# Performance work log

Measured on AMD Instinct MI355X. Metric: run time of the kernel, lower is better.

The kernel has to match this reference:

```python
import jax, jax.numpy as jnp
import numpy as np

EMBED_DIM = 1280
NUM_HEADS = 32
HEAD_DIM = EMBED_DIM // NUM_HEADS  # 40
SCALING = HEAD_DIM ** -0.5
BSZ, TGT_LEN, PAST_LEN = 2, 1024, 1024


def setup_inputs() -> dict:
    key = jax.random.key(0)
    ks = jax.random.split(key, 8)
    w_scale = 1.0 / np.sqrt(EMBED_DIM)
    return {
        "inputs": jax.random.normal(ks[0], (BSZ, TGT_LEN, EMBED_DIM), jnp.float32),
        "past_key": jax.random.normal(ks[1], (BSZ, NUM_HEADS, PAST_LEN, HEAD_DIM), jnp.float32),
        "past_value": jax.random.normal(ks[2], (BSZ, NUM_HEADS, PAST_LEN, HEAD_DIM), jnp.float32),
        "Wq": jax.random.normal(ks[3], (EMBED_DIM, EMBED_DIM), jnp.float32) * w_scale,
        "bq": jnp.zeros((EMBED_DIM,), jnp.float32),
        "Wk": jax.random.normal(ks[4], (EMBED_DIM, EMBED_DIM), jnp.float32) * w_scale,
        "bk": jnp.zeros((EMBED_DIM,), jnp.float32),
        "Wv": jax.random.normal(ks[5], (EMBED_DIM, EMBED_DIM), jnp.float32) * w_scale,
        "bv": jnp.zeros((EMBED_DIM,), jnp.float32),
        "Wo": jax.random.normal(ks[6], (EMBED_DIM, EMBED_DIM), jnp.float32) * w_scale,
        "bo": jnp.zeros((EMBED_DIM,), jnp.float32),
    }


def _shape(x, bsz):
    # [b, s, e] -> [b, h, s, d]
    return x.reshape(bsz, -1, NUM_HEADS, HEAD_DIM).transpose(0, 2, 1, 3)


def reference(inputs, past_key, past_value, Wq, bq, Wk, bk, Wv, bv, Wo, bo):
    bsz, tgt_len, _ = inputs.shape
    # projections (dropout rate is 0 -> identity)
    q = _shape((inputs @ Wq + bq) * SCALING, bsz)        # [b,h,t,d]
    k_new = _shape(inputs @ Wk + bk, bsz)                # [b,h,t,d]
    v_new = _shape(inputs @ Wv + bv, bsz)
    # KV-cache concat along seq axis
    key_states = jnp.concatenate([past_key, k_new], axis=2)    # [b,h,s,d]
    value_states = jnp.concatenate([past_value, v_new], axis=2)
    # attention: QK^T -> softmax -> AV (full score matrix, as original)
    attn_weights = jnp.einsum('bhid,bhjd->bhij', q, key_states)  # [b,h,t,s]
    attn_probs = jax.nn.softmax(attn_weights, axis=-1)
    attn_output = jnp.einsum('bhij,bhjd->bhid', attn_probs, value_states)  # [b,h,t,d]
    attn_output = attn_output.transpose(0, 2, 1, 3).reshape(bsz, tgt_len, EMBED_DIM)
    attn_output = attn_output @ Wo + bo
    return attn_output, key_states, value_states
```

## Files before the change

### kernel.cpp

```cpp
#include <hip/hip_runtime.h>
#include <hip/hip_bf16.h>

#define ED 1280
#define NH 32
#define HD 40
#define BSZ 2
#define TL 1024
#define SEQ 2048
#define SCALING 0.15811388300841897f

typedef __bf16 bf16x8 __attribute__((ext_vector_type(8)));
typedef float floatx4 __attribute__((ext_vector_type(4)));
typedef unsigned short ushort;
typedef ushort ushortx8 __attribute__((ext_vector_type(8)));

__device__ __forceinline__ ushort f2bf(float f) {
    __hip_bfloat16 h = __float2bfloat16(f);
    return *(ushort*)&h;
}
__device__ __forceinline__ unsigned pk2(float a, float b) {
    return (unsigned)f2bf(a) | ((unsigned)f2bf(b) << 16);
}

#define ASYNC16(g, l)                                                                 \
    __builtin_amdgcn_global_load_lds((const __attribute__((address_space(1))) void*)(g), \
                                     (__attribute__((address_space(3))) void*)(l), 16, 0, 0)

__global__ void convert_x_zero(const float* X, ushort* Xb, ushort* Qb) {
    int bid = blockIdx.x;
    if (bid < 2560) {
        int i = (bid * 256 + threadIdx.x) * 4;
        float4 v = *(const float4*)&X[i];
        ushort4 o;
        o.x = f2bf(v.x); o.y = f2bf(v.y); o.z = f2bf(v.z); o.w = f2bf(v.w);
        *(ushort4*)&Xb[i] = o;
    } else {
        int i = ((bid - 2560) * 256 + threadIdx.x) * 8;
        uint4 z = {0, 0, 0, 0};
        *(uint4*)&Qb[i] = z;
    }
}

__global__ void transpose_w(const float* w0, const float* w1,
                            const float* w2, const float* w3, ushort* wt) {
    __shared__ float tile[32][33];
    int z = blockIdx.z;
    const float* w = (z == 0) ? w0 : (z == 1) ? w1 : (z == 2) ? w2 : w3;
    ushort* o = wt + (size_t)z * ED * ED;
    int n0 = blockIdx.x * 32, k0 = blockIdx.y * 32;
    int tx = threadIdx.x, ty = threadIdx.y;
#pragma unroll
    for (int i = ty; i < 32; i += 8) tile[i][tx] = w[(k0 + i) * ED + n0 + tx];
    __syncthreads();
#pragma unroll
    for (int i = ty; i < 32; i += 8) o[(n0 + i) * ED + k0 + tx] = f2bf(tile[tx][i]);
}

__global__ void copy_past(const float* PK, const float* PV, float* keyOut, float* valOut) {
    int idx = blockIdx.x * 256 + threadIdx.x;
    int which = idx >= 655360;
    int f4 = which ? idx - 655360 : idx;
    const float4* src = (const float4*)(which ? PV : PK);
    float4* dst = (float4*)(which ? valOut : keyOut);
    int bhj = f4 / 10, c4 = f4 - bhj * 10;
    int bh = bhj >> 10, j = bhj & 1023;
    dst[(bh * SEQ + j) * 10 + c4] = src[f4];
}

__global__ void prep_k(const float* keyOut, ushort* Kb16) {
    int idx = blockIdx.x * 256 + threadIdx.x;
    int row = idx / 6, j = idx - row * 6;
    uint4 o = {0, 0, 0, 0};
    if (j < 5) {
        const float* s = &keyOut[(size_t)row * 40 + j * 8];
        float4 a = *(const float4*)s;
        float4 b = *(const float4*)(s + 4);
        o.x = pk2(a.x, a.y); o.y = pk2(a.z, a.w);
        o.z = pk2(b.x, b.y); o.w = pk2(b.z, b.w);
    }
    *(uint4*)&Kb16[(size_t)row * 48 + j * 8] = o;
}

__global__ void prep_v(const float* valOut, ushort* Vt16) {
    __shared__ ushort T[48 * 72];
    int bh = blockIdx.x, st = blockIdx.y;
    int tid = threadIdx.x;
    for (int i = tid; i < 8 * 72; i += 256) {
        int dr = i / 72, k = i - dr * 72;
        T[(40 + dr) * 72 + k] = (dr == 0) ? 0x3F80 : 0;
    }
    const float* src = valOut + ((size_t)bh * SEQ + st * 64) * 40;
    for (int i = tid; i < 640; i += 256) {
        int key = i / 10, c = i - key * 10;
        float4 v = *(const float4*)&src[key * 40 + c * 4];
        T[(c * 4 + 0) * 72 + key] = f2bf(v.x);
        T[(c * 4 + 1) * 72 + key] = f2bf(v.y);
        T[(c * 4 + 2) * 72 + key] = f2bf(v.z);
        T[(c * 4 + 3) * 72 + key] = f2bf(v.w);
    }
    __syncthreads();
    ushort* dst = Vt16 + (size_t)bh * 48 * 2048 + st * 64;
    for (int i = tid; i < 384; i += 256) {
        int d = i >> 3, c = i & 7;
        *(uint4*)&dst[(size_t)d * 2048 + c * 8] = *(const uint4*)&T[d * 72 + c * 8];
    }
}

__device__ __forceinline__ void gemm_core_db(const ushort* A, const ushort* Bt,
                                             ushort* As, ushort* Bs,
                                             int m0, int n0, floatx4 acc[4][2]) {
    int tidx = threadIdx.x;
    int wave = tidx >> 6, lane = tidx & 63;
    int wm = (wave >> 1) * 64, wn = (wave & 1) * 32;
    int fr = lane & 15, kq = lane >> 4;
    int fa = tidx * 8, ra = fa >> 5, ca = fa & 31;
    const ushort* a0 = &A[(m0 + ra) * ED + ca];
    const ushort* a1 = &A[(m0 + 64 + ra) * ED + ca];
    const ushort* bsrc = &Bt[(n0 + ra) * ED + ca];
    ASYNC16(a0, &As[fa]);
    ASYNC16(a1, &As[2048 + fa]);
    ASYNC16(bsrc, &Bs[fa]);
    __syncthreads();
    for (int k0 = 0; k0 < ED; k0 += 32) {
        int cur = (k0 >> 5) & 1;
        if (k0 + 32 < ED) {
            int nxt = cur ^ 1;
            ASYNC16(a0 + k0 + 32, &As[nxt * 4096 + fa]);
            ASYNC16(a1 + k0 + 32, &As[nxt * 4096 + 2048 + fa]);
            ASYNC16(bsrc + k0 + 32, &Bs[nxt * 2048 + fa]);
        }
        bf16x8 a[4], b[2];
#pragma unroll
        for (int mi = 0; mi < 4; ++mi)
            a[mi] = *(const bf16x8*)&As[cur * 4096 + (wm + mi * 16 + fr) * 32 + kq * 8];
#pragma unroll
        for (int ni = 0; ni < 2; ++ni)
            b[ni] = *(const bf16x8*)&Bs[cur * 2048 + (wn + ni * 16 + fr) * 32 + kq * 8];
#pragma unroll
        for (int mi = 0; mi < 4; ++mi)
#pragma unroll
            for (int ni = 0; ni < 2; ++ni)
                acc[mi][ni] = __builtin_amdgcn_mfma_f32_16x16x32_bf16(a[mi], b[ni], acc[mi][ni], 0, 0, 0);
        __syncthreads();
    }
}

__global__ __launch_bounds__(256) void gemm_qkv(const ushort* Xb, const ushort* Wt,
                                                const float* bq, const float* bk,
                                                const float* bv, ushort* Qb,
                                                float* keyOut, float* valOut) {
    __shared__ ushort As[2 * 128 * 32], Bs[2 * 64 * 32];
    int z = blockIdx.z;
    const ushort* Bt = Wt + (size_t)z * ED * ED;
    const float* bias = (z == 0) ? bq : (z == 1) ? bk : bv;
    int m0 = blockIdx.y * 128, n0 = blockIdx.x * 64;
    floatx4 acc[4][2] = {};
    gemm_core_db(Xb, Bt, As, Bs, m0, n0, acc);
    int lane = threadIdx.x & 63, wave = threadIdx.x >> 6;
    int wm = (wave >> 1) * 64, wn = (wave & 1) * 32;
    int cq = lane >> 4, cc = lane & 15;
#pragma unroll
    for (int mi = 0; mi < 4; ++mi)
#pragma unroll
        for (int ni = 0; ni < 2; ++ni) {
            int col = n0 + wn + ni * 16 + cc;
            float bvf = bias[col];
            int h = col / HD, dh = col - h * HD;
#pragma unroll
            for (int r = 0; r < 4; ++r) {
                int row = m0 + wm + mi * 16 + cq * 4 + r;
                int b = row >> 10, t = row & 1023;
                float v = acc[mi][ni][r] + bvf;
                if (z == 0) {
                    Qb[(((b * NH + h) * TL) + t) * 64 + dh] = f2bf(v * SCALING);
                } else {
                    int idx = ((b * NH + h) * SEQ + TL + t) * HD + dh;
                    (z == 1 ? keyOut : valOut)[idx] = v;
                }
            }
        }
}

__global__ __launch_bounds__(256) void gemm_out(const ushort* A, const ushort* Bt,
                                                const float* bias, float* out) {
    __shared__ ushort As[2 * 128 * 32], Bs[2 * 64 * 32];
    int m0 = blockIdx.y * 128, n0 = blockIdx.x * 64;
    floatx4 acc[4][2] = {};
    gemm_core_db(A, Bt, As, Bs, m0, n0, acc);
    int lane = threadIdx.x & 63, wave = threadIdx.x >> 6;
    int wm = (wave >> 1) * 64, wn = (wave & 1) * 32;
    int cq = lane >> 4, cc = lane & 15;
#pragma unroll
    for (int mi = 0; mi < 4; ++mi)
#pragma unroll
        for (int ni = 0; ni < 2; ++ni) {
            int col = n0 + wn + ni * 16 + cc;
            float bvf = bias[col];
#pragma unroll
            for (int r = 0; r < 4; ++r) {
                int row = m0 + wm + mi * 16 + cq * 4 + r;
                out[row * ED + col] = acc[mi][ni][r] + bvf;
            }
        }
}

__global__ __launch_bounds__(256) void attn_mfma(const ushort* Qb, const ushort* Kb16,
                                                 const ushort* Vt16, ushort* O) {
    __shared__ ushort Ks[2 * 64 * 64];
    __shared__ ushort Vs[2 * 48 * 64];

    int bh = blockIdx.x, b = bh >> 5, h = bh & 31;
    int tid = threadIdx.x, wave = tid >> 6, lane = tid & 63;
    int col = lane & 15, quad = lane >> 4;
    int qbase = blockIdx.y * 64 + wave * 16;

    bf16x8 qa[2];
#pragma unroll
    for (int ks = 0; ks < 2; ++ks)
        qa[ks] = *(const bf16x8*)(Qb + ((size_t)bh * TL + qbase + col) * 64 + ks * 32 + quad * 8);

    const ushort* ksrc[2];
    int kinc[2];
#pragma unroll
    for (int u = 0; u < 2; ++u) {
        int j = u * 256 + tid;
        int srow = j >> 3, ci = j & 7;
        int dch = ci ^ (srow & 7);
        int key = 32 * (srow >> 5) + 8 * ((srow >> 2) & 3) + 4 * ((srow >> 4) & 1) + (srow & 3);
        bool data = dch < 6;
        ksrc[u] = data ? Kb16 + ((size_t)bh * SEQ + key) * 48 + dch * 8 : Qb + 48;
        kinc[u] = data ? 64 * 48 : 0;
    }
    const ushort* vsrc[2];
#pragma unroll
    for (int u = 0; u < 2; ++u) {
        int j = u * 256 + tid;
        int row = j >> 3, ci = j & 7;
        int dch = ci ^ (row & 7);
        vsrc[u] = Vt16 + (size_t)bh * 48 * SEQ + (size_t)(row < 48 ? row : 0) * SEQ + dch * 8;
    }

    floatx4 Oacc[3] = {};
    int kxor = (col & 7) << 3;

#pragma unroll
    for (int u = 0; u < 2; ++u) {
        ASYNC16(ksrc[u], &Ks[(u * 256 + tid) * 8]);
        ksrc[u] += kinc[u];
    }
    ASYNC16(vsrc[0], &Vs[tid * 8]);
    vsrc[0] += 64;
    if (tid < 128) {
        ASYNC16(vsrc[1], &Vs[(256 + tid) * 8]);
        vsrc[1] += 64;
    }
    __syncthreads();

#pragma unroll 1
    for (int t = 0; t < SEQ / 64; ++t) {
        ushort* KsC = Ks + (t & 1) * (64 * 64);
        ushort* VsC = Vs + (t & 1) * (48 * 64);
        if (t + 1 < SEQ / 64) {
            ushort* KsN = Ks + ((t + 1) & 1) * (64 * 64);
            ushort* VsN = Vs + ((t + 1) & 1) * (48 * 64);
#pragma unroll
            for (int u = 0; u < 2; ++u) {
                ASYNC16(ksrc[u], &KsN[(u * 256 + tid) * 8]);
                ksrc[u] += kinc[u];
            }
            ASYNC16(vsrc[0], &VsN[tid * 8]);
            vsrc[0] += 64;
            if (tid < 128) {
                ASYNC16(vsrc[1], &VsN[(256 + tid) * 8]);
                vsrc[1] += 64;
            }
        }

        __builtin_amdgcn_s_setprio(1);
        floatx4 S[4] = {};
#pragma unroll
        for (int ks = 0; ks < 2; ++ks)
#pragma unroll
            for (int n = 0; n < 4; ++n) {
                int row = n * 16 + col;
                bf16x8 kb = *(const bf16x8*)&KsC[row * 64 + (((ks * 4 + quad) << 3) ^ kxor)];
                S[n] = __builtin_amdgcn_mfma_f32_16x16x32_bf16(kb, qa[ks], S[n], 0, 0, 0);
            }

#pragma unroll
        for (int ks = 0; ks < 2; ++ks) {
            unsigned w[4];
#pragma unroll
            for (int pi = 0; pi < 4; ++pi) {
                int i0 = pi * 2, i1 = i0 + 1;
                float s0 = S[2 * ks + (i0 >> 2)][i0 & 3];
                float s1 = S[2 * ks + (i1 >> 2)][i1 & 3];
                unsigned b0 = (unsigned)(int)fmaf(s0, 184.6649652f, 14035.0f);
                unsigned b1 = (unsigned)(int)fmaf(s1, 184.6649652f, 14035.0f);
                w[pi] = b0 | (b1 << 16);
            }
            uint4 pw;
            pw.x = w[0]; pw.y = w[1]; pw.z = w[2]; pw.w = w[3];
            bf16x8 pa = __builtin_bit_cast(bf16x8, pw);
            int c = ks * 4 + quad;
            int cpos = (c << 3) ^ kxor;
#pragma unroll
            for (int no = 0; no < 3; ++no) {
                int row = no * 16 + col;
                bf16x8 vb = *(const bf16x8*)&VsC[row * 64 + cpos];
                Oacc[no] = __builtin_amdgcn_mfma_f32_16x16x32_bf16(pa, vb, Oacc[no], 0, 0, 0);
            }
        }
        __builtin_amdgcn_s_setprio(0);

        __syncthreads();
    }

    float linv[4];
#pragma unroll
    for (int r = 0; r < 4; ++r)
        linv[r] = 1.f / __shfl(Oacc[2][r], (lane & 48) + 8, 64);
#pragma unroll
    for (int n = 0; n < 3; ++n) {
        int d = n * 16 + col;
        if (d < HD) {
#pragma unroll
            for (int r = 0; r < 4; ++r) {
                int q = qbase + quad * 4 + r;
                O[(size_t)(b * TL + q) * ED + h * HD + d] = f2bf(Oacc[n][r] * linv[r]);
            }
        }
    }
}

extern "C" void kernel_launch(void* const* d_in, const int* in_sizes, int n_in,
                              void* d_out, int out_size, void* d_ws, size_t ws_size,
                              hipStream_t stream) {
    const float* X  = (const float*)d_in[0];
    const float* PK = (const float*)d_in[1];
    const float* PV = (const float*)d_in[2];
    const float* Wq = (const float*)d_in[3];
    const float* bq = (const float*)d_in[4];
    const float* Wk = (const float*)d_in[5];
    const float* bk = (const float*)d_in[6];
    const float* Wv = (const float*)d_in[7];
    const float* bv = (const float*)d_in[8];
    const float* Wo = (const float*)d_in[9];
    const float* bo = (const float*)d_in[10];

    float* out = (float*)d_out;
    float* keyOut = out + 2621440;
    float* valOut = keyOut + 5242880;

    ushort* ws   = (ushort*)d_ws;
    ushort* Wt   = ws;
    ushort* Qb   = Wt + 4 * (ED * ED);
    ushort* Kb16 = Qb + (size_t)65536 * 64;
    ushort* Vt16 = Kb16 + (size_t)131072 * 48;
    ushort* Xb   = Vt16 + (size_t)64 * 48 * 2048;
    ushort* Aws  = Xb;

    convert_x_zero<<<dim3(4608), dim3(256), 0, stream>>>(X, Xb, Qb);
    transpose_w<<<dim3(40, 40, 4), dim3(32, 8), 0, stream>>>(Wq, Wk, Wv, Wo, Wt);
    copy_past<<<dim3(5120), dim3(256), 0, stream>>>(PK, PV, keyOut, valOut);
    gemm_qkv<<<dim3(20, 16, 3), dim3(256), 0, stream>>>(Xb, Wt, bq, bk, bv, Qb, keyOut, valOut);
    prep_k<<<dim3(3072), dim3(256), 0, stream>>>(keyOut, Kb16);
    prep_v<<<dim3(64, 32), dim3(256), 0, stream>>>(valOut, Vt16);
    attn_mfma<<<dim3(64, 16), dim3(256), 0, stream>>>(Qb, Kb16, Vt16, Aws);
    gemm_out<<<dim3(20, 16), dim3(256), 0, stream>>>(Aws, Wt + 3 * (ED * ED), bo, out);
}
```

Baseline: 240.1 us.

## Fuse past KV copy with bf16 K/V packing and emit new K/V from QKV GEMM

Replaces the separate copy_past, prep_k and prep_v kernels with one prep_past kernel. It copies the past key/value into the output cache and writes the bf16 padded K and transposed V buffers in the same pass. The QKV GEMM epilogue now also writes the new-token K rows and transposed V columns in bf16 directly. This removes two kernel launches and a re-read of the fp32 key/value caches, at the cost of extra scattered 2-byte stores in the GEMM epilogue.

```diff
diff --git a/kernel.cpp b/kernel.cpp
--- a/kernel.cpp
+++ b/kernel.cpp
@@ -17,9 +17,6 @@
 __device__ __forceinline__ ushort f2bf(float f) {
     __hip_bfloat16 h = __float2bfloat16(f);
     return *(ushort*)&h;
-}
-__device__ __forceinline__ unsigned pk2(float a, float b) {
-    return (unsigned)f2bf(a) | ((unsigned)f2bf(b) << 16);
 }
 
 #define ASYNC16(g, l)                                                                 \
@@ -56,53 +53,57 @@
     for (int i = ty; i < 32; i += 8) o[(n0 + i) * ED + k0 + tx] = f2bf(tile[tx][i]);
 }
 
-__global__ void copy_past(const float* PK, const float* PV, float* keyOut, float* valOut) {
-    int idx = blockIdx.x * 256 + threadIdx.x;
-    int which = idx >= 655360;
-    int f4 = which ? idx - 655360 : idx;
-    const float4* src = (const float4*)(which ? PV : PK);
-    float4* dst = (float4*)(which ? valOut : keyOut);
-    int bhj = f4 / 10, c4 = f4 - bhj * 10;
-    int bh = bhj >> 10, j = bhj & 1023;
-    dst[(bh * SEQ + j) * 10 + c4] = src[f4];
-}
-
-__global__ void prep_k(const float* keyOut, ushort* Kb16) {
-    int idx = blockIdx.x * 256 + threadIdx.x;
-    int row = idx / 6, j = idx - row * 6;
-    uint4 o = {0, 0, 0, 0};
-    if (j < 5) {
-        const float* s = &keyOut[(size_t)row * 40 + j * 8];
-        float4 a = *(const float4*)s;
-        float4 b = *(const float4*)(s + 4);
-        o.x = pk2(a.x, a.y); o.y = pk2(a.z, a.w);
-        o.z = pk2(b.x, b.y); o.w = pk2(b.z, b.w);
-    }
-    *(uint4*)&Kb16[(size_t)row * 48 + j * 8] = o;
-}
-
-__global__ void prep_v(const float* valOut, ushort* Vt16) {
+__global__ void prep_past(const float* PK, const float* PV,
+                          float* keyOut, float* valOut,
+                          ushort* Kb16, ushort* Vt16) {
     __shared__ ushort T[48 * 72];
     int bh = blockIdx.x, st = blockIdx.y;
     int tid = threadIdx.x;
+    int j0 = st * 64;
+    const float4* pk4 = (const float4*)PK;
+    const float4* pv4 = (const float4*)PV;
+    float4* ko4 = (float4*)keyOut;
+    float4* vo4 = (float4*)valOut;
+
     for (int i = tid; i < 8 * 72; i += 256) {
         int dr = i / 72, k = i - dr * 72;
         T[(40 + dr) * 72 + k] = (dr == 0) ? 0x3F80 : 0;
     }
-    const float* src = valOut + ((size_t)bh * SEQ + st * 64) * 40;
+
     for (int i = tid; i < 640; i += 256) {
         int key = i / 10, c = i - key * 10;
-        float4 v = *(const float4*)&src[key * 40 + c * 4];
+        float4 v = pk4[((size_t)bh * 1024 + j0 + key) * 10 + c];
+        ko4[((size_t)bh * 2048 + j0 + key) * 10 + c] = v;
+        ushort4 o;
+        o.x = f2bf(v.x); o.y = f2bf(v.y); o.z = f2bf(v.z); o.w = f2bf(v.w);
+        *(ushort4*)&Kb16[((size_t)bh * 2048 + j0 + key) * 48 + c * 4] = o;
+    }
+    if (tid < 64) {
+        uint4 z = {0, 0, 0, 0};
+        *(uint4*)&Kb16[((size_t)bh * 2048 + j0 + tid) * 48 + 40] = z;
+        *(uint4*)&Kb16[((size_t)bh * 2048 + 1024 + j0 + tid) * 48 + 40] = z;
+    }
+
+    for (int i = tid; i < 640; i += 256) {
+        int key = i / 10, c = i - key * 10;
+        float4 v = pv4[((size_t)bh * 1024 + j0 + key) * 10 + c];
+        vo4[((size_t)bh * 2048 + j0 + key) * 10 + c] = v;
         T[(c * 4 + 0) * 72 + key] = f2bf(v.x);
         T[(c * 4 + 1) * 72 + key] = f2bf(v.y);
         T[(c * 4 + 2) * 72 + key] = f2bf(v.z);
         T[(c * 4 + 3) * 72 + key] = f2bf(v.w);
     }
     __syncthreads();
-    ushort* dst = Vt16 + (size_t)bh * 48 * 2048 + st * 64;
+    ushort* dst = Vt16 + (size_t)bh * 48 * 2048 + j0;
     for (int i = tid; i < 384; i += 256) {
         int d = i >> 3, c = i & 7;
         *(uint4*)&dst[(size_t)d * 2048 + c * 8] = *(const uint4*)&T[d * 72 + c * 8];
+    }
+    if (tid < 64) {
+        int d = 40 + (tid >> 3), c = tid & 7;
+        unsigned f = (d == 40) ? 0x3F803F80u : 0u;
+        uint4 z4; z4.x = f; z4.y = f; z4.z = f; z4.w = f;
+        *(uint4*)&Vt16[(size_t)bh * 48 * 2048 + (size_t)d * 2048 + 1024 + j0 + c * 8] = z4;
     }
 }
 
@@ -148,7 +149,8 @@
 __global__ __launch_bounds__(256) void gemm_qkv(const ushort* Xb, const ushort* Wt,
                                                 const float* bq, const float* bk,
                                                 const float* bv, ushort* Qb,
-                                                float* keyOut, float* valOut) {
+                                                float* keyOut, float* valOut,
+                                                ushort* Kb16, ushort* Vt16) {
     __shared__ ushort As[2 * 128 * 32], Bs[2 * 64 * 32];
     int z = blockIdx.z;
     const ushort* Bt = Wt + (size_t)z * ED * ED;
@@ -166,18 +168,26 @@
             int col = n0 + wn + ni * 16 + cc;
             float bvf = bias[col];
             int h = col / HD, dh = col - h * HD;
+            int row0 = m0 + wm + mi * 16 + cq * 4;
+            int b0 = row0 >> 10, t0 = row0 & 1023;
+            int bh = b0 * NH + h;
+            ushort4 vt;
 #pragma unroll
             for (int r = 0; r < 4; ++r) {
-                int row = m0 + wm + mi * 16 + cq * 4 + r;
-                int b = row >> 10, t = row & 1023;
                 float v = acc[mi][ni][r] + bvf;
                 if (z == 0) {
-                    Qb[(((b * NH + h) * TL) + t) * 64 + dh] = f2bf(v * SCALING);
+                    Qb[((size_t)bh * TL + t0 + r) * 64 + dh] = f2bf(v * SCALING);
                 } else {
-                    int idx = ((b * NH + h) * SEQ + TL + t) * HD + dh;
+                    int idx = (bh * SEQ + TL + t0 + r) * HD + dh;
                     (z == 1 ? keyOut : valOut)[idx] = v;
+                    if (z == 1)
+                        Kb16[((size_t)bh * SEQ + TL + t0 + r) * 48 + dh] = f2bf(v);
+                    else
+                        ((ushort*)&vt)[r] = f2bf(v);
                 }
             }
+            if (z == 2)
+                *(ushort4*)&Vt16[((size_t)bh * 48 + dh) * 2048 + TL + t0] = vt;
         }
 }
 
@@ -362,10 +372,9 @@
 
     convert_x_zero<<<dim3(4608), dim3(256), 0, stream>>>(X, Xb, Qb);
     transpose_w<<<dim3(40, 40, 4), dim3(32, 8), 0, stream>>>(Wq, Wk, Wv, Wo, Wt);
-    copy_past<<<dim3(5120), dim3(256), 0, stream>>>(PK, PV, keyOut, valOut);
-    gemm_qkv<<<dim3(20, 16, 3), dim3(256), 0, stream>>>(Xb, Wt, bq, bk, bv, Qb, keyOut, valOut);
-    prep_k<<<dim3(3072), dim3(256), 0, stream>>>(keyOut, Kb16);
-    prep_v<<<dim3(64, 32), dim3(256), 0, stream>>>(valOut, Vt16);
+    prep_past<<<dim3(64, 16), dim3(256), 0, stream>>>(PK, PV, keyOut, valOut, Kb16, Vt16);
+    gemm_qkv<<<dim3(20, 16, 3), dim3(256), 0, stream>>>(Xb, Wt, bq, bk, bv, Qb,
+                                                        keyOut, valOut, Kb16, Vt16);
     attn_mfma<<<dim3(64, 16), dim3(256), 0, stream>>>(Qb, Kb16, Vt16, Aws);
     gemm_out<<<dim3(20, 16), dim3(256), 0, stream>>>(Aws, Wt + 3 * (ED * ED), bo, out);
 }
```

New measurement: 236.0 us. No clear change (-1.7%).
